# Optimization experiments

Hardware: AMD Instinct MI355X
Metric: run time of the kernel (lower is better)

The kernel has to match this reference:

```python
import jax, jax.numpy as jnp
import numpy as np

B, D, H, T = 4096, 1024, 1024, 50
FREE_RATIO = 0.0  # default free_running_ratio


def setup_inputs() -> dict:
    key = jax.random.key(0)
    ks = jax.random.split(key, 10)
    s_init = 1.0 / np.sqrt(D)
    s_gru = 1.0 / np.sqrt(H)
    return {
        "ev_context": jax.random.normal(ks[0], (B, D), dtype=jnp.float32),
        "teacher_deltas": jax.random.normal(ks[1], (B, T, 2), dtype=jnp.float32),
        "w_init": jax.random.uniform(ks[2], (H, D), jnp.float32, -s_init, s_init),
        "b_init": jax.random.uniform(ks[3], (H,), jnp.float32, -s_init, s_init),
        "w_ih": jax.random.uniform(ks[4], (3 * H, 2), jnp.float32, -s_gru, s_gru),
        "w_hh": jax.random.uniform(ks[5], (3 * H, H), jnp.float32, -s_gru, s_gru),
        "b_ih": jax.random.uniform(ks[6], (3 * H,), jnp.float32, -s_gru, s_gru),
        "b_hh": jax.random.uniform(ks[7], (3 * H,), jnp.float32, -s_gru, s_gru),
        "w_out": jax.random.uniform(ks[8], (2, H), jnp.float32, -s_gru, s_gru),
        "b_out": jax.random.uniform(ks[9], (2,), jnp.float32, -s_gru, s_gru),
    }


def reference(ev_context, teacher_deltas, w_init, b_init, w_ih, w_hh, b_ih, b_hh, w_out, b_out):
    # h0 = tanh(Linear(ev_context))  -> (B, H)
    h0 = jnp.tanh(ev_context @ w_init.T + b_init)
    prev0 = jnp.zeros((B, 2), dtype=ev_context.dtype)
    # teacher forcing mask: rand(B) < free_running_ratio, drawn per step
    free_mask = jax.random.uniform(jax.random.key(1), (T, B)) < FREE_RATIO
    teach_seq = jnp.swapaxes(teacher_deltas, 0, 1)  # (T, B, 2)

    def step(carry, xs):
        h, prev = carry
        teach_t, free_t = xs
        # PyTorch GRU cell, gate order (r, z, n)
        gx = prev @ w_ih.T + b_ih            # (B, 3H)
        gh = h @ w_hh.T + b_hh               # (B, 3H)
        xr, xz, xn = jnp.split(gx, 3, axis=-1)
        hr, hz, hn = jnp.split(gh, 3, axis=-1)
        r = jax.nn.sigmoid(xr + hr)
        z = jax.nn.sigmoid(xz + hz)
        n = jnp.tanh(xn + r * hn)
        h_new = (1.0 - z) * n + z * h
        delta = h_new @ w_out.T + b_out      # (B, 2)
        prev_next = jnp.where(free_t[:, None], delta, teach_t)
        return (h_new, prev_next), delta

    _, deltas = jax.lax.scan(step, (h0, prev0), (teach_seq, free_mask))
    pred_deltas = jnp.swapaxes(deltas, 0, 1)          # (B, T, 2)
    pred_pos = jnp.cumsum(pred_deltas, axis=1)        # (B, T, 2)
    return pred_deltas, pred_pos
```

## Files before the change

kernel.cpp:

```cpp
#include <hip/hip_runtime.h>
#include <math.h>

#define B_SZ 4096
#define D_SZ 1024
#define H_SZ 1024
#define T_SZ 50

typedef _Float16 f16;
typedef __attribute__((ext_vector_type(8))) _Float16 f16x8;
typedef __attribute__((ext_vector_type(4))) _Float16 f16x4;
typedef __attribute__((ext_vector_type(2))) _Float16 f16x2;
typedef __attribute__((ext_vector_type(4))) float f32x4;
typedef __attribute__((ext_vector_type(4))) float f4;

__device__ __forceinline__ float fast_sigmoid(float x) {
    return 1.0f / (1.0f + __expf(-x));
}
__device__ __forceinline__ float fast_tanh(float x) {
    return 1.0f - 2.0f / (__expf(2.0f * x) + 1.0f);
}

__device__ __forceinline__ void gl_lds16(const void* g, void* l) {
    __builtin_amdgcn_global_load_lds(
        (const __attribute__((address_space(1))) unsigned int*)g,
        (__attribute__((address_space(3))) unsigned int*)l, 16, 0, 0);
}

#define LGKM0() do { asm volatile("s_waitcnt lgkmcnt(0)" ::: "memory"); __builtin_amdgcn_sched_barrier(0); } while (0)

__global__ __launch_bounds__(256) void conv_kernel(
        const float* __restrict__ s, f16* __restrict__ d, int n) {
    int i = (blockIdx.x * 256 + threadIdx.x) * 4;
    if (i < n) {
        f4 v = *(const f4*)&s[i];
        f16x4 o = {(f16)v[0], (f16)v[1], (f16)v[2], (f16)v[3]};
        *(f16x4*)&d[i] = o;
    }
}

__global__ __launch_bounds__(256) void ttrans_kernel(
        const float* __restrict__ teach, f16* __restrict__ tT) {
    int idx = blockIdx.x * 256 + threadIdx.x;
    if (idx >= T_SZ * B_SZ) return;
    int t = idx >> 12, b = idx & 4095;
    float v0 = teach[b * (T_SZ * 2) + t * 2 + 0];
    float v1 = teach[b * (T_SZ * 2) + t * 2 + 1];
    f16x2 o = {(f16)v0, (f16)v1};
    *(f16x2*)&tT[(size_t)idx * 2] = o;
}

__global__ __launch_bounds__(256) void prepack_kernel(
        const float* __restrict__ w, f16* __restrict__ wpk) {
    const int idx = blockIdx.x * 256 + threadIdx.x;
    const int kt = blockIdx.y, jb = blockIdx.z;
    const int row = idx >> 2, s = idx & 3;
    const int g = row >> 6, jj = row & 63;
    const int col = (kt << 5) + ((s ^ ((row >> 1) & 3)) << 3);
    const float* src =
        w + ((size_t)(g << 10) + (jb << 6) + jj) * H_SZ + col;
    f4 v0 = *(const f4*)src;
    f4 v1 = *(const f4*)(src + 4);
    f16x8 o = {(f16)v0[0], (f16)v0[1], (f16)v0[2], (f16)v0[3],
               (f16)v1[0], (f16)v1[1], (f16)v1[2], (f16)v1[3]};
    *(f16x8*)&wpk[((size_t)jb * 32 + kt) * 6144 + idx * 8] = o;
}

__global__ __launch_bounds__(256, 2) void h0_kernel(
        const f16* __restrict__ ev, const f16* __restrict__ wi,
        const float* __restrict__ b_init, f16* __restrict__ hh) {
    __shared__ __align__(16) f16 lds[6144];
    const int tid = threadIdx.x;
    const int lane = tid & 63, wave = tid >> 6;
    const int b0 = blockIdx.y * 128, j0 = blockIdx.x * 64;
    const int wm = wave >> 1, wn = wave & 1;
    const int lrow = lane & 15, quad = lane >> 4;

    const f16* gsrc[3];
    int lbase[3];
    {
        const int row16 = lane >> 2, part = lane & 3;
#pragma unroll
        for (int i = 0; i < 3; ++i) {
            int c = wave + 4 * i;
            if (c < 8) {
                gsrc[i] = ev + (size_t)(b0 + c * 16 + row16) * D_SZ + part * 8;
                lbase[i] = c * 512;
            } else {
                int cc = c - 8;
                gsrc[i] = wi + (size_t)(j0 + cc * 16 + row16) * D_SZ + part * 8;
                lbase[i] = 4096 + cc * 512;
            }
        }
    }

    int offA[4], offB[2];
#pragma unroll
    for (int mi = 0; mi < 4; ++mi)
        offA[mi] = (wm * 64 + mi * 16 + lrow) * 32 + quad * 8;
#pragma unroll
    for (int ni = 0; ni < 2; ++ni)
        offB[ni] = 4096 + (wn * 32 + ni * 16 + lrow) * 32 + quad * 8;

    f32x4 acc[4][2] = {};

    for (int k0 = 0; k0 < D_SZ; k0 += 32) {
        __syncthreads();
#pragma unroll
        for (int i = 0; i < 3; ++i)
            gl_lds16(gsrc[i] + k0, &lds[lbase[i]] + lane * 8);
        __syncthreads();
        f16x8 aa[4], bb[2];
#pragma unroll
        for (int mi = 0; mi < 4; ++mi) aa[mi] = *(const f16x8*)&lds[offA[mi]];
#pragma unroll
        for (int ni = 0; ni < 2; ++ni) bb[ni] = *(const f16x8*)&lds[offB[ni]];
#pragma unroll
        for (int mi = 0; mi < 4; ++mi)
#pragma unroll
            for (int ni = 0; ni < 2; ++ni)
                acc[mi][ni] = __builtin_amdgcn_mfma_f32_16x16x32_f16(
                    aa[mi], bb[ni], acc[mi][ni], 0, 0, 0);
    }

#pragma unroll
    for (int ni = 0; ni < 2; ++ni) {
        const int j = j0 + wn * 32 + ni * 16 + lrow;
        const float bj = b_init[j];
#pragma unroll
        for (int mi = 0; mi < 4; ++mi)
#pragma unroll
            for (int reg = 0; reg < 4; ++reg) {
                const int b = b0 + wm * 64 + mi * 16 + quad * 4 + reg;
                hh[(size_t)b * H_SZ + j] = (f16)tanhf(acc[mi][ni][reg] + bj);
            }
    }
}

__global__ __launch_bounds__(256, 2) void step_kernel(
        const f16* __restrict__ hh, const f16* __restrict__ wpk,
        const float* __restrict__ b_hh, const float* __restrict__ w_ih,
        const float* __restrict__ b_ih, const float* __restrict__ w_out,
        const f16* __restrict__ tT, f16* __restrict__ nhh,
        float* __restrict__ out, const float* __restrict__ partP,
        float* __restrict__ partC, int step_t) {
    constexpr int TILE_E = 10240;
    __shared__ __align__(16) f16 lds[4 * TILE_E];
    const int tid = threadIdx.x;
    const int lane = tid & 63, wave = tid >> 6;
    const int wm = wave >> 1, wn = wave & 1;
    const int id = blockIdx.x;
    const int xcd = id & 7, slot = id >> 3;
    const int bx = (xcd & 1) * 8 + (slot & 7);
    const int by = (xcd >> 1) * 8 + (slot >> 3);
    const int b0 = by * 128, j0 = bx * 64;
    const int lrow = lane & 15, quad = lane >> 4;

    if (step_t > 0 && tid < 16) {
        const int b = b0 + bx * 8 + (tid >> 1), cc = tid & 1;
        float s = 0.f;
#pragma unroll
        for (int x = 0; x < 16; ++x) s += partP[x * 8192 + b * 2 + cc];
        out[b * (T_SZ * 2) + (step_t - 1) * 2 + cc] = s;
    }

    const f16* ga[2];
    const f16* gb;
    {
        const int r = tid >> 2;
        const int cs = ((tid & 3) ^ ((tid >> 3) & 3)) * 8;
#pragma unroll
        for (int i = 0; i < 2; ++i)
            ga[i] = hh + (size_t)(b0 + i * 64 + r) * H_SZ + cs;
        gb = wpk + (size_t)bx * (32 * 6144);
    }
    auto issueT = [&](int kt) {
        const int sb = (kt & 3) * TILE_E;
#pragma unroll
        for (int i = 0; i < 2; ++i)
            gl_lds16(ga[i] + kt * 32, &lds[sb + i * 2048 + tid * 8]);
#pragma unroll
        for (int i = 0; i < 3; ++i)
            gl_lds16(gb + kt * 6144 + i * 2048 + tid * 8,
                     &lds[sb + 4096 + i * 2048 + tid * 8]);
    };

    const int swz = (quad ^ ((lrow >> 1) & 3)) * 8;
    int offA[4], offB[6];
#pragma unroll
    for (int mi = 0; mi < 4; ++mi)
        offA[mi] = (wm * 64 + mi * 16 + lrow) * 32 + swz;
#pragma unroll
    for (int f = 0; f < 6; ++f)
        offB[f] = 4096 + ((f >> 1) * 64 + wn * 32 + (f & 1) * 16 + lrow) * 32 + swz;

    f32x4 acc[3][4][2] = {};

    issueT(0);
    issueT(1);
    issueT(2);

    for (int tt = 0; tt < 32; ++tt) {
        if (tt < 30)       asm volatile("s_waitcnt vmcnt(10)" ::: "memory");
        else if (tt == 30) asm volatile("s_waitcnt vmcnt(5)" ::: "memory");
        else               asm volatile("s_waitcnt vmcnt(0)" ::: "memory");
        __builtin_amdgcn_s_barrier();
        asm volatile("" ::: "memory");
        const int rb = (tt & 3) * TILE_E;
        f16x8 aa[4], bv[6];
#pragma unroll
        for (int mi = 0; mi < 4; ++mi)
            aa[mi] = *(const f16x8*)&lds[rb + offA[mi]];
#pragma unroll
        for (int f = 0; f < 6; ++f)
            bv[f] = *(const f16x8*)&lds[rb + offB[f]];
        if (tt < 29) issueT(tt + 3);
        LGKM0();
        __builtin_amdgcn_s_setprio(1);
#pragma unroll
        for (int f = 0; f < 6; ++f) {
            const int g = f >> 1, ni = f & 1;
#pragma unroll
            for (int mi = 0; mi < 4; ++mi)
                acc[g][mi][ni] = __builtin_amdgcn_mfma_f32_16x16x32_f16(
                    aa[mi], bv[f], acc[g][mi][ni], 0, 0, 0);
        }
        __builtin_amdgcn_s_setprio(0);
    }

    float p0[4][4], p1[4][4];
#pragma unroll
    for (int mi = 0; mi < 4; ++mi)
#pragma unroll
        for (int reg = 0; reg < 4; ++reg) {
            const int b = b0 + wm * 64 + mi * 16 + quad * 4 + reg;
            if (step_t > 0) {
                f16x2 tv = *(const f16x2*)&tT[((size_t)(step_t - 1) * B_SZ + b) * 2];
                p0[mi][reg] = (float)tv[0];
                p1[mi][reg] = (float)tv[1];
            } else {
                p0[mi][reg] = 0.f;
                p1[mi][reg] = 0.f;
            }
        }

    float s0[4][4] = {}, s1[4][4] = {};
#pragma unroll
    for (int ni = 0; ni < 2; ++ni) {
        const int j = j0 + wn * 32 + ni * 16 + lrow;
        const float wr0 = w_ih[(0 * H_SZ + j) * 2 + 0];
        const float wr1 = w_ih[(0 * H_SZ + j) * 2 + 1];
        const float wz0 = w_ih[(1 * H_SZ + j) * 2 + 0];
        const float wz1 = w_ih[(1 * H_SZ + j) * 2 + 1];
        const float wn0 = w_ih[(2 * H_SZ + j) * 2 + 0];
        const float wn1 = w_ih[(2 * H_SZ + j) * 2 + 1];
        const float br = b_ih[0 * H_SZ + j] + b_hh[0 * H_SZ + j];
        const float bz = b_ih[1 * H_SZ + j] + b_hh[1 * H_SZ + j];
        const float bn = b_ih[2 * H_SZ + j];
        const float hbn = b_hh[2 * H_SZ + j];
        const float wo0 = w_out[j], wo1 = w_out[H_SZ + j];
#pragma unroll
        for (int mi = 0; mi < 4; ++mi) {
#pragma unroll
            for (int reg = 0; reg < 4; ++reg) {
                const int b = b0 + wm * 64 + mi * 16 + quad * 4 + reg;
                const float hr = acc[0][mi][ni][reg];
                const float hz = acc[1][mi][ni][reg];
                const float hn_ = acc[2][mi][ni][reg] + hbn;
                const float xr = wr0 * p0[mi][reg] + wr1 * p1[mi][reg] + br;
                const float xz = wz0 * p0[mi][reg] + wz1 * p1[mi][reg] + bz;
                const float xn = wn0 * p0[mi][reg] + wn1 * p1[mi][reg] + bn;
                const float r = fast_sigmoid(xr + hr);
                const float z = fast_sigmoid(xz + hz);
                const float n = fast_tanh(xn + r * hn_);
                const size_t idx = (size_t)b * H_SZ + j;
                const float hold = (float)hh[idx];
                const float hnew = (1.0f - z) * n + z * hold;
                nhh[idx] = (f16)hnew;
                s0[mi][reg] += hnew * wo0;
                s1[mi][reg] += hnew * wo1;
            }
        }
    }

    float ra[4][4], rc[4][4];
#pragma unroll
    for (int mi = 0; mi < 4; ++mi)
#pragma unroll
        for (int reg = 0; reg < 4; ++reg) {
            float a = s0[mi][reg], c = s1[mi][reg];
#pragma unroll
            for (int m = 1; m < 16; m <<= 1) {
                a += __shfl_xor(a, m);
                c += __shfl_xor(c, m);
            }
            ra[mi][reg] = a;
            rc[mi][reg] = c;
        }
    float* red = (float*)lds;
    __syncthreads();
    if (wn == 1 && lrow == 0) {
#pragma unroll
        for (int mi = 0; mi < 4; ++mi)
#pragma unroll
            for (int reg = 0; reg < 4; ++reg) {
                const int key = wm * 64 + mi * 16 + quad * 4 + reg;
                red[key * 2 + 0] = ra[mi][reg];
                red[key * 2 + 1] = rc[mi][reg];
            }
    }
    __syncthreads();
    if (wn == 0 && lrow == 0) {
#pragma unroll
        for (int mi = 0; mi < 4; ++mi)
#pragma unroll
            for (int reg = 0; reg < 4; ++reg) {
                const int key = wm * 64 + mi * 16 + quad * 4 + reg;
                const int b = b0 + key;
                partC[bx * 8192 + b * 2 + 0] = ra[mi][reg] + red[key * 2 + 0];
                partC[bx * 8192 + b * 2 + 1] = rc[mi][reg] + red[key * 2 + 1];
            }
    }
}

__global__ __launch_bounds__(256) void final_kernel(
        float* __restrict__ out, float* __restrict__ pos,
        const float* __restrict__ b_out, const float* __restrict__ partLast) {
    int idx = blockIdx.x * 256 + threadIdx.x;
    if (idx >= B_SZ * 2) return;
    int b = idx >> 1, c = idx & 1;
    float bc = b_out[c];
    float acc = 0.0f;
    for (int t = 0; t < T_SZ - 1; ++t) {
        float d = out[b * (T_SZ * 2) + t * 2 + c] + bc;
        out[b * (T_SZ * 2) + t * 2 + c] = d;
        acc += d;
        pos[b * (T_SZ * 2) + t * 2 + c] = acc;
    }
    float s = 0.f;
#pragma unroll
    for (int x = 0; x < 16; ++x) s += partLast[x * 8192 + b * 2 + c];
    float d = s + bc;
    out[b * (T_SZ * 2) + (T_SZ - 1) * 2 + c] = d;
    acc += d;
    pos[b * (T_SZ * 2) + (T_SZ - 1) * 2 + c] = acc;
}

extern "C" void kernel_launch(void* const* d_in, const int* in_sizes, int n_in,
                              void* d_out, int out_size, void* d_ws, size_t ws_size,
                              hipStream_t stream) {
    const float* ev     = (const float*)d_in[0];
    const float* teach  = (const float*)d_in[1];
    const float* w_init = (const float*)d_in[2];
    const float* b_init = (const float*)d_in[3];
    const float* w_ih   = (const float*)d_in[4];
    const float* w_hh   = (const float*)d_in[5];
    const float* b_ih   = (const float*)d_in[6];
    const float* b_hh   = (const float*)d_in[7];
    const float* w_out  = (const float*)d_in[8];
    const float* b_out  = (const float*)d_in[9];

    float* out = (float*)d_out;
    float* pos = out + (size_t)B_SZ * T_SZ * 2;

    f16* ws = (f16*)d_ws;
    f16* hA    = ws;
    f16* hB    = hA + (size_t)B_SZ * H_SZ;
    f16* wpk   = hB + (size_t)B_SZ * H_SZ;
    f16* winit = wpk + (size_t)3 * H_SZ * H_SZ;
    f16* evf   = hB;
    f16* tT    = winit;
    float* pA  = (float*)(winit + 417792);
    float* pB  = pA + 131072;

    conv_kernel<<<(H_SZ * D_SZ) / 1024, 256, 0, stream>>>(w_init, winit, H_SZ * D_SZ);
    conv_kernel<<<(B_SZ * D_SZ) / 1024, 256, 0, stream>>>(ev, evf, B_SZ * D_SZ);
    prepack_kernel<<<dim3(3, 32, 16), 256, 0, stream>>>(w_hh, wpk);

    dim3 g0(H_SZ / 64, B_SZ / 128);
    h0_kernel<<<g0, 256, 0, stream>>>(evf, winit, b_init, hA);

    ttrans_kernel<<<(T_SZ * B_SZ + 255) / 256, 256, 0, stream>>>(teach, tT);

    f16 *hc = hA, *hn = hB;
    for (int t = 0; t < T_SZ; ++t) {
        float* partC = (t & 1) ? pB : pA;
        float* partP = (t & 1) ? pA : pB;
        step_kernel<<<512, 256, 0, stream>>>(hc, wpk, b_hh, w_ih, b_ih, w_out,
                                             tT, hn, out, partP, partC, t);
        f16* tmp = hc; hc = hn; hn = tmp;
    }
    final_kernel<<<(B_SZ * 2 + 255) / 256, 256, 0, stream>>>(out, pos, b_out, pB);
}
```

Measured before the change: 1.923 ms.

## Double-buffer LDS fragment reads to overlap with MFMA in GRU step GEMM

Restructures the K-loop of the per-step recurrent GEMM so fragments for the next K tile are loaded from LDS into a second register set while the MFMAs for the current tile run. The loop is unrolled by two with an explicit prologue and epilogue, and the barrier and global-to-LDS issue order is rearranged. This aims to hide LDS read latency behind matrix-core work. In exchange it doubles the fragment registers, which could lower occupancy, and the waitcnt/barrier sequencing is more delicate.

```diff
diff --git a/kernel.cpp b/kernel.cpp
--- a/kernel.cpp
+++ b/kernel.cpp
@@ -27,6 +27,7 @@
 }
 
 #define LGKM0() do { asm volatile("s_waitcnt lgkmcnt(0)" ::: "memory"); __builtin_amdgcn_sched_barrier(0); } while (0)
+#define BARX() do { __builtin_amdgcn_s_barrier(); asm volatile("" ::: "memory"); } while (0)
 
 __global__ __launch_bounds__(256) void conv_kernel(
         const float* __restrict__ s, f16* __restrict__ d, int n) {
@@ -194,38 +195,78 @@
         offB[f] = 4096 + ((f >> 1) * 64 + wn * 32 + (f & 1) * 16 + lrow) * 32 + swz;
 
     f32x4 acc[3][4][2] = {};
+    f16x8 aa[2][4], bv[2][6];
+
+#define RDFRAG(S, BUFC) do {                                             \
+        const int rb_ = (BUFC) * TILE_E;                                 \
+        _Pragma("unroll")                                                \
+        for (int mi = 0; mi < 4; ++mi)                                   \
+            aa[S][mi] = *(const f16x8*)&lds[rb_ + offA[mi]];             \
+        _Pragma("unroll")                                                \
+        for (int f = 0; f < 6; ++f)                                      \
+            bv[S][f] = *(const f16x8*)&lds[rb_ + offB[f]];               \
+    } while (0)
+
+#define MFMA24(S) do {                                                   \
+        __builtin_amdgcn_s_setprio(1);                                   \
+        _Pragma("unroll")                                                \
+        for (int f = 0; f < 6; ++f) {                                    \
+            const int g = f >> 1, ni = f & 1;                            \
+            _Pragma("unroll")                                            \
+            for (int mi = 0; mi < 4; ++mi)                               \
+                acc[g][mi][ni] = __builtin_amdgcn_mfma_f32_16x16x32_f16( \
+                    aa[S][mi], bv[S][f], acc[g][mi][ni], 0, 0, 0);       \
+        }                                                                \
+        __builtin_amdgcn_s_setprio(0);                                   \
+    } while (0)
 
     issueT(0);
     issueT(1);
     issueT(2);
-
-    for (int tt = 0; tt < 32; ++tt) {
-        if (tt < 30)       asm volatile("s_waitcnt vmcnt(10)" ::: "memory");
-        else if (tt == 30) asm volatile("s_waitcnt vmcnt(5)" ::: "memory");
-        else               asm volatile("s_waitcnt vmcnt(0)" ::: "memory");
-        __builtin_amdgcn_s_barrier();
-        asm volatile("" ::: "memory");
-        const int rb = (tt & 3) * TILE_E;
-        f16x8 aa[4], bv[6];
-#pragma unroll
-        for (int mi = 0; mi < 4; ++mi)
-            aa[mi] = *(const f16x8*)&lds[rb + offA[mi]];
-#pragma unroll
-        for (int f = 0; f < 6; ++f)
-            bv[f] = *(const f16x8*)&lds[rb + offB[f]];
-        if (tt < 29) issueT(tt + 3);
+    asm volatile("s_waitcnt vmcnt(10)" ::: "memory");
+    BARX();
+    RDFRAG(0, 0);
+    LGKM0();
+
+    for (int tt = 0; tt < 28; tt += 2) {
+        BARX();
+        issueT(tt + 3);
+        asm volatile("s_waitcnt vmcnt(10)" ::: "memory");
+        RDFRAG(1, (tt + 1) & 3);
+        __builtin_amdgcn_sched_barrier(0);
+        MFMA24(0);
         LGKM0();
-        __builtin_amdgcn_s_setprio(1);
-#pragma unroll
-        for (int f = 0; f < 6; ++f) {
-            const int g = f >> 1, ni = f & 1;
-#pragma unroll
-            for (int mi = 0; mi < 4; ++mi)
-                acc[g][mi][ni] = __builtin_amdgcn_mfma_f32_16x16x32_f16(
-                    aa[mi], bv[f], acc[g][mi][ni], 0, 0, 0);
-        }
-        __builtin_amdgcn_s_setprio(0);
-    }
+        BARX();
+        issueT(tt + 4);
+        asm volatile("s_waitcnt vmcnt(10)" ::: "memory");
+        RDFRAG(0, (tt + 2) & 3);
+        __builtin_amdgcn_sched_barrier(0);
+        MFMA24(1);
+        LGKM0();
+    }
+    BARX();
+    issueT(31);
+    asm volatile("s_waitcnt vmcnt(10)" ::: "memory");
+    RDFRAG(1, 29 & 3);
+    __builtin_amdgcn_sched_barrier(0);
+    MFMA24(0);
+    LGKM0();
+    BARX();
+    asm volatile("s_waitcnt vmcnt(5)" ::: "memory");
+    RDFRAG(0, 30 & 3);
+    __builtin_amdgcn_sched_barrier(0);
+    MFMA24(1);
+    LGKM0();
+    BARX();
+    asm volatile("s_waitcnt vmcnt(0)" ::: "memory");
+    RDFRAG(1, 31 & 3);
+    __builtin_amdgcn_sched_barrier(0);
+    MFMA24(0);
+    LGKM0();
+    MFMA24(1);
+
+#undef RDFRAG
+#undef MFMA24
 
     float p0[4][4], p1[4][4];
 #pragma unroll
```

Result: no change. 1.940 ms (+0.9%).

## Switch GRU step GEMM to 32x32x16 MFMA and remap block-to-XCD tiling

Applied to the files above, without the earlier changes.

Replaces the 16x16x32 f16 MFMA tiles in the recurrent step kernel with 32x32x16 MFMA tiles, rewriting the LDS fragment offsets, the accumulator layout and the epilogue indexing to match the new output layout. The larger MFMA shape is meant to cut LDS fragment reads per FLOP and raise matrix-core throughput. The block-to-XCD mapping is also changed so each XCD owns whole batch rows across all column tiles, which should improve L2 reuse of the hidden-state tile. In exchange, the epilogue shuffle reduction now runs over 32 lanes, and the new register and index mapping must be exactly right.

```diff
diff --git a/kernel.cpp b/kernel.cpp
--- a/kernel.cpp
+++ b/kernel.cpp
@@ -11,6 +11,7 @@
 typedef __attribute__((ext_vector_type(4))) _Float16 f16x4;
 typedef __attribute__((ext_vector_type(2))) _Float16 f16x2;
 typedef __attribute__((ext_vector_type(4))) float f32x4;
+typedef __attribute__((ext_vector_type(16))) float f32x16;
 typedef __attribute__((ext_vector_type(4))) float f4;
 
 __device__ __forceinline__ float fast_sigmoid(float x) {
@@ -27,6 +28,7 @@
 }
 
 #define LGKM0() do { asm volatile("s_waitcnt lgkmcnt(0)" ::: "memory"); __builtin_amdgcn_sched_barrier(0); } while (0)
+#define BARX() do { __builtin_amdgcn_s_barrier(); asm volatile("" ::: "memory"); } while (0)
 
 __global__ __launch_bounds__(256) void conv_kernel(
         const float* __restrict__ s, f16* __restrict__ d, int n) {
@@ -150,10 +152,11 @@
     const int wm = wave >> 1, wn = wave & 1;
     const int id = blockIdx.x;
     const int xcd = id & 7, slot = id >> 3;
-    const int bx = (xcd & 1) * 8 + (slot & 7);
-    const int by = (xcd >> 1) * 8 + (slot >> 3);
+    const int by = xcd * 4 + (slot >> 4);
+    const int bx = slot & 15;
     const int b0 = by * 128, j0 = bx * 64;
-    const int lrow = lane & 15, quad = lane >> 4;
+    const int l31 = lane & 31, hi = lane >> 5;
+    const int sw4 = (l31 >> 1) & 3;
 
     if (step_t > 0 && tid < 16) {
         const int b = b0 + bx * 8 + (tid >> 1), cc = tid & 1;
@@ -184,16 +187,21 @@
                      &lds[sb + 4096 + i * 2048 + tid * 8]);
     };
 
-    const int swz = (quad ^ ((lrow >> 1) & 3)) * 8;
-    int offA[4], offB[6];
-#pragma unroll
-    for (int mi = 0; mi < 4; ++mi)
-        offA[mi] = (wm * 64 + mi * 16 + lrow) * 32 + swz;
-#pragma unroll
-    for (int f = 0; f < 6; ++f)
-        offB[f] = 4096 + ((f >> 1) * 64 + wn * 32 + (f & 1) * 16 + lrow) * 32 + swz;
-
-    f32x4 acc[3][4][2] = {};
+    int offA[2][2], offB[3][2];
+#pragma unroll
+    for (int mi = 0; mi < 2; ++mi)
+#pragma unroll
+        for (int kh = 0; kh < 2; ++kh)
+            offA[mi][kh] = (wm * 64 + mi * 32 + l31) * 32 +
+                           (((kh * 2 + hi) ^ sw4) * 8);
+#pragma unroll
+    for (int g = 0; g < 3; ++g)
+#pragma unroll
+        for (int kh = 0; kh < 2; ++kh)
+            offB[g][kh] = 4096 + (g * 64 + wn * 32 + l31) * 32 +
+                          (((kh * 2 + hi) ^ sw4) * 8);
+
+    f32x16 acc[3][2] = {};
 
     issueT(0);
     issueT(1);
@@ -206,115 +214,99 @@
         __builtin_amdgcn_s_barrier();
         asm volatile("" ::: "memory");
         const int rb = (tt & 3) * TILE_E;
-        f16x8 aa[4], bv[6];
-#pragma unroll
-        for (int mi = 0; mi < 4; ++mi)
-            aa[mi] = *(const f16x8*)&lds[rb + offA[mi]];
-#pragma unroll
-        for (int f = 0; f < 6; ++f)
-            bv[f] = *(const f16x8*)&lds[rb + offB[f]];
+        f16x8 aa[2][2], bb[3][2];
+#pragma unroll
+        for (int mi = 0; mi < 2; ++mi)
+#pragma unroll
+            for (int kh = 0; kh < 2; ++kh)
+                aa[mi][kh] = *(const f16x8*)&lds[rb + offA[mi][kh]];
+#pragma unroll
+        for (int g = 0; g < 3; ++g)
+#pragma unroll
+            for (int kh = 0; kh < 2; ++kh)
+                bb[g][kh] = *(const f16x8*)&lds[rb + offB[g][kh]];
         if (tt < 29) issueT(tt + 3);
         LGKM0();
         __builtin_amdgcn_s_setprio(1);
 #pragma unroll
-        for (int f = 0; f < 6; ++f) {
-            const int g = f >> 1, ni = f & 1;
-#pragma unroll
-            for (int mi = 0; mi < 4; ++mi)
-                acc[g][mi][ni] = __builtin_amdgcn_mfma_f32_16x16x32_f16(
-                    aa[mi], bv[f], acc[g][mi][ni], 0, 0, 0);
-        }
+        for (int kh = 0; kh < 2; ++kh)
+#pragma unroll
+            for (int g = 0; g < 3; ++g)
+#pragma unroll
+                for (int mi = 0; mi < 2; ++mi)
+                    acc[g][mi] = __builtin_amdgcn_mfma_f32_32x32x16_f16(
+                        aa[mi][kh], bb[g][kh], acc[g][mi], 0, 0, 0);
         __builtin_amdgcn_s_setprio(0);
     }
 
-    float p0[4][4], p1[4][4];
-#pragma unroll
-    for (int mi = 0; mi < 4; ++mi)
-#pragma unroll
-        for (int reg = 0; reg < 4; ++reg) {
-            const int b = b0 + wm * 64 + mi * 16 + quad * 4 + reg;
+    const int j = j0 + wn * 32 + l31;
+    const float wr0 = w_ih[(0 * H_SZ + j) * 2 + 0];
+    const float wr1 = w_ih[(0 * H_SZ + j) * 2 + 1];
+    const float wz0 = w_ih[(1 * H_SZ + j) * 2 + 0];
+    const float wz1 = w_ih[(1 * H_SZ + j) * 2 + 1];
+    const float wn0 = w_ih[(2 * H_SZ + j) * 2 + 0];
+    const float wn1 = w_ih[(2 * H_SZ + j) * 2 + 1];
+    const float br = b_ih[0 * H_SZ + j] + b_hh[0 * H_SZ + j];
+    const float bz = b_ih[1 * H_SZ + j] + b_hh[1 * H_SZ + j];
+    const float bn = b_ih[2 * H_SZ + j];
+    const float hbn = b_hh[2 * H_SZ + j];
+    const float wo0 = w_out[j], wo1 = w_out[H_SZ + j];
+
+    float ra[2][16], rc[2][16];
+#pragma unroll
+    for (int mi = 0; mi < 2; ++mi) {
+#pragma unroll
+        for (int reg = 0; reg < 16; ++reg) {
+            const int b = b0 + wm * 64 + mi * 32 + (reg & 3) + 8 * (reg >> 2) + 4 * hi;
+            float tp0 = 0.f, tp1 = 0.f;
             if (step_t > 0) {
                 f16x2 tv = *(const f16x2*)&tT[((size_t)(step_t - 1) * B_SZ + b) * 2];
-                p0[mi][reg] = (float)tv[0];
-                p1[mi][reg] = (float)tv[1];
-            } else {
-                p0[mi][reg] = 0.f;
-                p1[mi][reg] = 0.f;
-            }
-        }
-
-    float s0[4][4] = {}, s1[4][4] = {};
-#pragma unroll
-    for (int ni = 0; ni < 2; ++ni) {
-        const int j = j0 + wn * 32 + ni * 16 + lrow;
-        const float wr0 = w_ih[(0 * H_SZ + j) * 2 + 0];
-        const float wr1 = w_ih[(0 * H_SZ + j) * 2 + 1];
-        const float wz0 = w_ih[(1 * H_SZ + j) * 2 + 0];
-        const float wz1 = w_ih[(1 * H_SZ + j) * 2 + 1];
-        const float wn0 = w_ih[(2 * H_SZ + j) * 2 + 0];
-        const float wn1 = w_ih[(2 * H_SZ + j) * 2 + 1];
-        const float br = b_ih[0 * H_SZ + j] + b_hh[0 * H_SZ + j];
-        const float bz = b_ih[1 * H_SZ + j] + b_hh[1 * H_SZ + j];
-        const float bn = b_ih[2 * H_SZ + j];
-        const float hbn = b_hh[2 * H_SZ + j];
-        const float wo0 = w_out[j], wo1 = w_out[H_SZ + j];
-#pragma unroll
-        for (int mi = 0; mi < 4; ++mi) {
-#pragma unroll
-            for (int reg = 0; reg < 4; ++reg) {
-                const int b = b0 + wm * 64 + mi * 16 + quad * 4 + reg;
-                const float hr = acc[0][mi][ni][reg];
-                const float hz = acc[1][mi][ni][reg];
-                const float hn_ = acc[2][mi][ni][reg] + hbn;
-                const float xr = wr0 * p0[mi][reg] + wr1 * p1[mi][reg] + br;
-                const float xz = wz0 * p0[mi][reg] + wz1 * p1[mi][reg] + bz;
-                const float xn = wn0 * p0[mi][reg] + wn1 * p1[mi][reg] + bn;
-                const float r = fast_sigmoid(xr + hr);
-                const float z = fast_sigmoid(xz + hz);
-                const float n = fast_tanh(xn + r * hn_);
-                const size_t idx = (size_t)b * H_SZ + j;
-                const float hold = (float)hh[idx];
-                const float hnew = (1.0f - z) * n + z * hold;
-                nhh[idx] = (f16)hnew;
-                s0[mi][reg] += hnew * wo0;
-                s1[mi][reg] += hnew * wo1;
-            }
-        }
-    }
-
-    float ra[4][4], rc[4][4];
-#pragma unroll
-    for (int mi = 0; mi < 4; ++mi)
-#pragma unroll
-        for (int reg = 0; reg < 4; ++reg) {
-            float a = s0[mi][reg], c = s1[mi][reg];
-#pragma unroll
-            for (int m = 1; m < 16; m <<= 1) {
+                tp0 = (float)tv[0];
+                tp1 = (float)tv[1];
+            }
+            const float hr = acc[0][mi][reg];
+            const float hz = acc[1][mi][reg];
+            const float hn_ = acc[2][mi][reg] + hbn;
+            const float xr = wr0 * tp0 + wr1 * tp1 + br;
+            const float xz = wz0 * tp0 + wz1 * tp1 + bz;
+            const float xn = wn0 * tp0 + wn1 * tp1 + bn;
+            const float r = fast_sigmoid(xr + hr);
+            const float z = fast_sigmoid(xz + hz);
+            const float n = fast_tanh(xn + r * hn_);
+            const size_t idx = (size_t)b * H_SZ + j;
+            const float hold = (float)hh[idx];
+            const float hnew = (1.0f - z) * n + z * hold;
+            nhh[idx] = (f16)hnew;
+            float a = hnew * wo0, c = hnew * wo1;
+#pragma unroll
+            for (int m = 1; m < 32; m <<= 1) {
                 a += __shfl_xor(a, m);
                 c += __shfl_xor(c, m);
             }
             ra[mi][reg] = a;
             rc[mi][reg] = c;
         }
+    }
+
     float* red = (float*)lds;
     __syncthreads();
-    if (wn == 1 && lrow == 0) {
-#pragma unroll
-        for (int mi = 0; mi < 4; ++mi)
-#pragma unroll
-            for (int reg = 0; reg < 4; ++reg) {
-                const int key = wm * 64 + mi * 16 + quad * 4 + reg;
+    if (wn == 1 && l31 == 0) {
+#pragma unroll
+        for (int mi = 0; mi < 2; ++mi)
+#pragma unroll
+            for (int reg = 0; reg < 16; ++reg) {
+                const int key = wm * 64 + mi * 32 + (reg & 3) + 8 * (reg >> 2) + 4 * hi;
                 red[key * 2 + 0] = ra[mi][reg];
                 red[key * 2 + 1] = rc[mi][reg];
             }
     }
     __syncthreads();
-    if (wn == 0 && lrow == 0) {
-#pragma unroll
-        for (int mi = 0; mi < 4; ++mi)
-#pragma unroll
-            for (int reg = 0; reg < 4; ++reg) {
-                const int key = wm * 64 + mi * 16 + quad * 4 + reg;
+    if (wn == 0 && l31 == 0) {
+#pragma unroll
+        for (int mi = 0; mi < 2; ++mi)
+#pragma unroll
+            for (int reg = 0; reg < 16; ++reg) {
+                const int key = wm * 64 + mi * 32 + (reg & 3) + 8 * (reg >> 2) + 4 * hi;
                 const int b = b0 + key;
                 partC[bx * 8192 + b * 2 + 0] = ra[mi][reg] + red[key * 2 + 0];
                 partC[bx * 8192 + b * 2 + 1] = rc[mi][reg] + red[key * 2 + 1];
```

After: 2.473 ms. 28.6% more time.

## Load GRU recurrent weights directly to registers, bypassing LDS

Applied to the files above, without the earlier changes.

The packed W_hh tiles are now read by each wave straight from global memory into registers, double-buffered across two register banks. Only the hidden-state A tiles still go through LDS via async global-to-LDS copies, which shrinks the LDS footprint per block. The prepack drops its XOR swizzle because B no longer passes through LDS. This trades LDS traffic and capacity for duplicated global and L2 reads of W across the two M-waves, plus more vector registers and a hand-tuned vmcnt schedule that could be fragile.

```diff
diff --git a/kernel.cpp b/kernel.cpp
--- a/kernel.cpp
+++ b/kernel.cpp
@@ -27,6 +27,7 @@
 }
 
 #define LGKM0() do { asm volatile("s_waitcnt lgkmcnt(0)" ::: "memory"); __builtin_amdgcn_sched_barrier(0); } while (0)
+#define BARX() do { __builtin_amdgcn_s_barrier(); asm volatile("" ::: "memory"); } while (0)
 
 __global__ __launch_bounds__(256) void conv_kernel(
         const float* __restrict__ s, f16* __restrict__ d, int n) {
@@ -55,7 +56,7 @@
     const int kt = blockIdx.y, jb = blockIdx.z;
     const int row = idx >> 2, s = idx & 3;
     const int g = row >> 6, jj = row & 63;
-    const int col = (kt << 5) + ((s ^ ((row >> 1) & 3)) << 3);
+    const int col = (kt << 5) + (s << 3);
     const float* src =
         w + ((size_t)(g << 10) + (jb << 6) + jj) * H_SZ + col;
     f4 v0 = *(const f4*)src;
@@ -143,7 +144,7 @@
         const f16* __restrict__ tT, f16* __restrict__ nhh,
         float* __restrict__ out, const float* __restrict__ partP,
         float* __restrict__ partC, int step_t) {
-    constexpr int TILE_E = 10240;
+    constexpr int TILE_E = 4096;
     __shared__ __align__(16) f16 lds[4 * TILE_E];
     const int tid = threadIdx.x;
     const int lane = tid & 63, wave = tid >> 6;
@@ -164,68 +165,114 @@
     }
 
     const f16* ga[2];
-    const f16* gb;
     {
         const int r = tid >> 2;
         const int cs = ((tid & 3) ^ ((tid >> 3) & 3)) * 8;
 #pragma unroll
         for (int i = 0; i < 2; ++i)
             ga[i] = hh + (size_t)(b0 + i * 64 + r) * H_SZ + cs;
-        gb = wpk + (size_t)bx * (32 * 6144);
-    }
-    auto issueT = [&](int kt) {
+    }
+    auto issueA = [&](int kt) {
         const int sb = (kt & 3) * TILE_E;
 #pragma unroll
         for (int i = 0; i < 2; ++i)
             gl_lds16(ga[i] + kt * 32, &lds[sb + i * 2048 + tid * 8]);
-#pragma unroll
-        for (int i = 0; i < 3; ++i)
-            gl_lds16(gb + kt * 6144 + i * 2048 + tid * 8,
-                     &lds[sb + 4096 + i * 2048 + tid * 8]);
     };
 
+    const f16* bp[6];
+    {
+        const f16* wt = wpk + (size_t)bx * (32 * 6144);
+#pragma unroll
+        for (int f = 0; f < 6; ++f) {
+            const int row = (f >> 1) * 64 + wn * 32 + (f & 1) * 16 + lrow;
+            bp[f] = wt + row * 32 + quad * 8;
+        }
+    }
+    f16x8 bbA[6], bbB[6];
+
+#define LOADB(BANK, KT) do {                                             \
+        _Pragma("unroll")                                                \
+        for (int f = 0; f < 6; ++f)                                      \
+            bb##BANK[f] = *(const f16x8*)(bp[f] + (size_t)(KT) * 6144);  \
+    } while (0)
+
     const int swz = (quad ^ ((lrow >> 1) & 3)) * 8;
-    int offA[4], offB[6];
+    int offA[4];
 #pragma unroll
     for (int mi = 0; mi < 4; ++mi)
         offA[mi] = (wm * 64 + mi * 16 + lrow) * 32 + swz;
-#pragma unroll
-    for (int f = 0; f < 6; ++f)
-        offB[f] = 4096 + ((f >> 1) * 64 + wn * 32 + (f & 1) * 16 + lrow) * 32 + swz;
 
     f32x4 acc[3][4][2] = {};
 
-    issueT(0);
-    issueT(1);
-    issueT(2);
-
-    for (int tt = 0; tt < 32; ++tt) {
-        if (tt < 30)       asm volatile("s_waitcnt vmcnt(10)" ::: "memory");
-        else if (tt == 30) asm volatile("s_waitcnt vmcnt(5)" ::: "memory");
-        else               asm volatile("s_waitcnt vmcnt(0)" ::: "memory");
-        __builtin_amdgcn_s_barrier();
-        asm volatile("" ::: "memory");
-        const int rb = (tt & 3) * TILE_E;
-        f16x8 aa[4], bv[6];
+#define MFMA24(BANK) do {                                                \
+        __builtin_amdgcn_s_setprio(1);                                   \
+        _Pragma("unroll")                                                \
+        for (int f = 0; f < 6; ++f) {                                    \
+            const int g = f >> 1, ni = f & 1;                            \
+            _Pragma("unroll")                                            \
+            for (int mi = 0; mi < 4; ++mi)                               \
+                acc[g][mi][ni] = __builtin_amdgcn_mfma_f32_16x16x32_f16( \
+                    aa[mi], bb##BANK[f], acc[g][mi][ni], 0, 0, 0);       \
+        }                                                                \
+        __builtin_amdgcn_s_setprio(0);                                   \
+    } while (0)
+
+    issueA(0);
+    issueA(1);
+    LOADB(A, 0);
+    issueA(2);
+    LOADB(B, 1);
+
+    f16x8 aa[4];
+    for (int tt = 0; tt < 30; tt += 2) {
+        asm volatile("s_waitcnt vmcnt(8)" ::: "memory");
+        BARX();
+        {
+            const int rb = (tt & 3) * TILE_E;
+#pragma unroll
+            for (int mi = 0; mi < 4; ++mi)
+                aa[mi] = *(const f16x8*)&lds[rb + offA[mi]];
+        }
+        if (tt < 29) issueA(tt + 3);
+        LGKM0();
+        MFMA24(A);
+        LOADB(A, tt + 2);
+        asm volatile("s_waitcnt vmcnt(8)" ::: "memory");
+        BARX();
+        {
+            const int rb = ((tt + 1) & 3) * TILE_E;
+#pragma unroll
+            for (int mi = 0; mi < 4; ++mi)
+                aa[mi] = *(const f16x8*)&lds[rb + offA[mi]];
+        }
+        if (tt + 1 < 29) issueA(tt + 4);
+        LGKM0();
+        MFMA24(B);
+        if (tt + 1 <= 29) LOADB(B, tt + 3);
+    }
+    asm volatile("s_waitcnt vmcnt(6)" ::: "memory");
+    BARX();
+    {
+        const int rb = (30 & 3) * TILE_E;
 #pragma unroll
         for (int mi = 0; mi < 4; ++mi)
             aa[mi] = *(const f16x8*)&lds[rb + offA[mi]];
-#pragma unroll
-        for (int f = 0; f < 6; ++f)
-            bv[f] = *(const f16x8*)&lds[rb + offB[f]];
-        if (tt < 29) issueT(tt + 3);
-        LGKM0();
-        __builtin_amdgcn_s_setprio(1);
-#pragma unroll
-        for (int f = 0; f < 6; ++f) {
-            const int g = f >> 1, ni = f & 1;
-#pragma unroll
-            for (int mi = 0; mi < 4; ++mi)
-                acc[g][mi][ni] = __builtin_amdgcn_mfma_f32_16x16x32_f16(
-                    aa[mi], bv[f], acc[g][mi][ni], 0, 0, 0);
-        }
-        __builtin_amdgcn_s_setprio(0);
-    }
+    }
+    LGKM0();
+    MFMA24(A);
+    asm volatile("s_waitcnt vmcnt(0)" ::: "memory");
+    BARX();
+    {
+        const int rb = (31 & 3) * TILE_E;
+#pragma unroll
+        for (int mi = 0; mi < 4; ++mi)
+            aa[mi] = *(const f16x8*)&lds[rb + offA[mi]];
+    }
+    LGKM0();
+    MFMA24(B);
+
+#undef LOADB
+#undef MFMA24
 
     float p0[4][4], p1[4][4];
 #pragma unroll
```

Measured after the change: 2.227 ms. 15.8% more time.
